# Kernel tuning notes

Measured on AMD Instinct MI355X. Metric: run time of the kernel, lower is better.

Reference implementation:

```python
import jax, jax.numpy as jnp
import numpy as np

_PI = np.pi

def _fibonacci_sphere(n):
    i = np.arange(n, dtype=np.float64)
    y = 1.0 - (i / float(n - 1)) * 2.0
    r = np.sqrt(np.maximum(1.0 - y * y, 0.0))
    theta = _PI * (3.0 - np.sqrt(5.0)) * i
    return np.stack([np.cos(theta) * r, y, np.sin(theta) * r], -1).astype(np.float32)

def _normalize(v, eps=1e-12):
    n = jnp.linalg.norm(v, axis=-1, keepdims=True)
    return v / jnp.maximum(n, eps)

def _sh4(v):
    # l=4 real spherical harmonics, orthonormal ('integral') normalization, 9 comps m=-4..4
    v = _normalize(v)
    x, y, z = v[..., 0], v[..., 1], v[..., 2]
    x2, y2, z2 = x * x, y * y, z * z
    c_m4 = 0.75 * np.sqrt(35.0 / _PI)
    c_m3 = 0.75 * np.sqrt(35.0 / (2.0 * _PI))
    c_m2 = 0.75 * np.sqrt(5.0 / _PI)
    c_m1 = 0.75 * np.sqrt(5.0 / (2.0 * _PI))
    c_0  = (3.0 / 16.0) * np.sqrt(1.0 / _PI)
    c_p2 = (3.0 / 8.0) * np.sqrt(5.0 / _PI)
    c_p4 = (3.0 / 16.0) * np.sqrt(35.0 / _PI)
    return jnp.stack([
        c_m4 * x * y * (x2 - y2),
        c_m3 * y * z * (3.0 * x2 - y2),
        c_m2 * x * y * (7.0 * z2 - 1.0),
        c_m1 * y * z * (7.0 * z2 - 3.0),
        c_0 * (35.0 * z2 * z2 - 30.0 * z2 + 3.0),
        c_m1 * x * z * (7.0 * z2 - 3.0),
        c_p2 * (x2 - y2) * (7.0 * z2 - 1.0),
        c_m3 * x * z * (x2 - y2),
        c_p4 * (x2 * x2 - 6.0 * x2 * y2 + y2 * y2),
    ], axis=-1)

def _matrix_to_quaternion(m):
    # pytorch3d-style robust conversion, m: [..., 3, 3], returns (w, x, y, z)
    m00, m01, m02 = m[..., 0, 0], m[..., 0, 1], m[..., 0, 2]
    m10, m11, m12 = m[..., 1, 0], m[..., 1, 1], m[..., 1, 2]
    m20, m21, m22 = m[..., 2, 0], m[..., 2, 1], m[..., 2, 2]
    q_abs = jnp.sqrt(jnp.maximum(jnp.stack([
        1.0 + m00 + m11 + m22,
        1.0 + m00 - m11 - m22,
        1.0 - m00 + m11 - m22,
        1.0 - m00 - m11 + m22,
    ], -1), 0.0))
    c0 = jnp.stack([q_abs[..., 0] ** 2, m21 - m12, m02 - m20, m10 - m01], -1)
    c1 = jnp.stack([m21 - m12, q_abs[..., 1] ** 2, m10 + m01, m02 + m20], -1)
    c2 = jnp.stack([m02 - m20, m10 + m01, q_abs[..., 2] ** 2, m12 + m21], -1)
    c3 = jnp.stack([m10 - m01, m20 + m02, m21 + m12, q_abs[..., 3] ** 2], -1)
    cand = jnp.stack([c0, c1, c2, c3], -2) / (2.0 * jnp.maximum(q_abs, 0.1))[..., None]
    best = jnp.argmax(q_abs, axis=-1)
    return jnp.take_along_axis(cand, best[..., None, None], axis=-2)[..., 0, :]

def setup_inputs() -> dict:
    key = jax.random.key(0)
    k0, k1, k4, k6 = jax.random.split(key, 4)
    B = 16384
    return {
        "f0": jax.random.normal(k0, (B, 1), dtype=jnp.float32),
        "f1": jax.random.normal(k1, (B, 3), dtype=jnp.float32),
        "f4": jax.random.normal(k4, (B, 9), dtype=jnp.float32),
        "f6": jax.random.normal(k6, (B, 13), dtype=jnp.float32),
        "grid_vecs": jnp.asarray(_fibonacci_sphere(10000)),
    }

def reference(f0, f1, f4, f6, grid_vecs):
    Y4 = _sh4(grid_vecs)                               # [G, 9]
    signal = jnp.einsum('bi,gi->bg', f4, Y4)           # [B, G]  (memory-bound skinny matmul)
    z_idx = jnp.argmax(signal, axis=1)
    z_axis = grid_vecs[z_idx]                          # [B, 3]
    dots = jnp.einsum('bi,gi->bg', z_axis, grid_vecs)  # [B, G]
    masked = jnp.where(jnp.abs(dots) < 0.2, signal, -jnp.inf)
    x_idx = jnp.argmax(masked, axis=1)
    x_axis = grid_vecs[x_idx]
    z_axis = _normalize(z_axis)
    proj = jnp.sum(x_axis * z_axis, -1, keepdims=True) * z_axis
    x_axis = _normalize(x_axis - proj)
    y_axis = jnp.cross(z_axis, x_axis)
    R = jnp.stack([x_axis, y_axis, z_axis], axis=-1)   # axes as columns
    q_rec = _matrix_to_quaternion(R)                   # [B, 4]
    boundary_map = f0 * (180.0 / _PI)
    return q_rec, boundary_map
```

## Files before the change

kernel.cpp:

```cpp
#include <hip/hip_runtime.h>
#include <math.h>
#include <stdint.h>

#define NB 16384
#define NG 10000
#define NGT 313
#define NCH 20
#define MAXTPC 16

typedef _Float16 half4 __attribute__((ext_vector_type(4)));
typedef _Float16 half8 __attribute__((ext_vector_type(8)));
typedef float    floatx16 __attribute__((ext_vector_type(16)));

#define ROWMAP(r, kh) (((r) & 3) + 8 * ((r) >> 2) + 4 * (kh))

__device__ inline float max3f(float a, float b, float c) {
    float d;
    asm("v_max3_f32 %0, %1, %2, %3" : "=v"(d) : "v"(a), "v"(b), "v"(c));
    return d;
}

#define PACKF(p_, c_, F_) \
    asm("v_and_or_b32 %0, %1, %2, " F_ : "=v"(p_) : "v"(c_), "s"(mskc))

__device__ inline void stage_sh(const float* __restrict__ gv, half4* lds4, int t0, int nt) {
    const int nrows = nt * 32;
    for (int lr = threadIdx.x; lr < nrows; lr += 256) {
        int g = t0 * 32 + lr;
        half4 s0, s1, s2, s3;
        if (g >= NG) {
            const _Float16 qn = (_Float16)__builtin_nanf("");
            s0 = (half4){qn, qn, qn, qn}; s1 = s0; s2 = s0; s3 = s0;
        } else {
            float x = gv[3 * g + 0], y = gv[3 * g + 1], z = gv[3 * g + 2];
            float n2 = x * x + y * y + z * z;
            float rn = __frsqrt_rn(fmaxf(n2, 1e-24f));
            float vx = x * rn, vy = y * rn, vz = z * rn;
            float x2 = vx * vx, y2 = vy * vy, z2 = vz * vz;
            const float c_m4 = (float)(0.75 * sqrt(35.0 / M_PI));
            const float c_m3 = (float)(0.75 * sqrt(35.0 / (2.0 * M_PI)));
            const float c_m2 = (float)(0.75 * sqrt(5.0 / M_PI));
            const float c_m1 = (float)(0.75 * sqrt(5.0 / (2.0 * M_PI)));
            const float c_0  = (float)((3.0 / 16.0) * sqrt(1.0 / M_PI));
            const float c_p2 = (float)((3.0 / 8.0) * sqrt(5.0 / M_PI));
            const float c_p4 = (float)((3.0 / 16.0) * sqrt(35.0 / M_PI));
            s0[0] = (_Float16)(c_m4 * vx * vy * (x2 - y2));
            s0[1] = (_Float16)(c_m3 * vy * vz * (3.0f * x2 - y2));
            s0[2] = (_Float16)(c_m2 * vx * vy * (7.0f * z2 - 1.0f));
            s0[3] = (_Float16)(c_m1 * vy * vz * (7.0f * z2 - 3.0f));
            s1[0] = (_Float16)(c_0  * (35.0f * z2 * z2 - 30.0f * z2 + 3.0f));
            s1[1] = (_Float16)(c_m1 * vx * vz * (7.0f * z2 - 3.0f));
            s1[2] = (_Float16)(c_p2 * (x2 - y2) * (7.0f * z2 - 1.0f));
            s1[3] = (_Float16)(c_m3 * vx * vz * (x2 - y2));
            s2[0] = (_Float16)(c_p4 * (x2 * x2 - 6.0f * x2 * y2 + y2 * y2));
            s2[1] = (_Float16)x;
            s2[2] = (_Float16)y;
            s2[3] = (_Float16)z;
            s3 = (half4){0, 0, 0, 0};
        }
        half4* row = lds4 + lr * 5;
        row[0] = s0; row[1] = s1; row[2] = s2; row[3] = s3;
    }
}

__device__ inline half8 make_bfrag(const float* __restrict__ f4, int b, int kh) {
    half8 a = {0, 0, 0, 0, 0, 0, 0, 0};
    const float* fr = f4 + (size_t)b * 9;
    if (kh == 0) {
#pragma unroll
        for (int j = 0; j < 8; ++j) a[j] = (_Float16)fr[j];
    } else {
        a[0] = (_Float16)fr[8];
    }
    return a;
}

__device__ inline void merge_vg(float& v, int& g, float v2, int g2) {
    bool take = (v2 > v) || (v2 == v && g2 < g);
    v = take ? v2 : v;
    g = take ? g2 : g;
}

__global__ __launch_bounds__(256, 6) void k_pass1(const float* __restrict__ f4,
                                                  const float* __restrict__ gv,
                                                  float* __restrict__ Pv,
                                                  int* __restrict__ Pi) {
    __shared__ half4 lds4[MAXTPC * 32 * 5];
    const int lane = threadIdx.x & 63;
    const int w = threadIdx.x >> 6;
    const int W = blockIdx.x * 4 + w;
    const int n = lane & 31, kh = lane >> 5;
    const int chunk = blockIdx.y;
    const int b = W * 32 + n;

    const int t0 = (NGT * chunk) / NCH;
    const int t1 = (NGT * (chunk + 1)) / NCH;
    const int nt = t1 - t0;

    stage_sh(gv, lds4, t0, nt);
    const half8 bf = make_bfrag(f4, b, kh);
    __syncthreads();

    const floatx16 zero16 = {0.f,0.f,0.f,0.f, 0.f,0.f,0.f,0.f, 0.f,0.f,0.f,0.f, 0.f,0.f,0.f,0.f};
    const unsigned mskc = 0xFFFFFFF0u;
    float run = -INFINITY; int bt = 0;

    const half4* lp = lds4 + n * 5 + kh * 2;
    half4 a0 = lp[0], a1 = lp[1]; lp += 32 * 5;

    for (int t = 0; t < nt - 1; ++t) {
        half4 b0 = lp[0], b1 = lp[1]; lp += 32 * 5;
        half8 af = __builtin_shufflevector(a0, a1, 0, 1, 2, 3, 4, 5, 6, 7);
        floatx16 c = __builtin_amdgcn_mfma_f32_32x32x16_f16(af, bf, zero16, 0, 0, 0);
        float p0,p1,p2,p3,p4,p5,p6,p7,p8,p9,p10,p11,p12,p13,p14,p15;
        PACKF(p0,  c[0],  "15"); PACKF(p1,  c[1],  "14");
        PACKF(p2,  c[2],  "13"); PACKF(p3,  c[3],  "12");
        PACKF(p4,  c[4],  "11"); PACKF(p5,  c[5],  "10");
        PACKF(p6,  c[6],  "9");  PACKF(p7,  c[7],  "8");
        PACKF(p8,  c[8],  "7");  PACKF(p9,  c[9],  "6");
        PACKF(p10, c[10], "5");  PACKF(p11, c[11], "4");
        PACKF(p12, c[12], "3");  PACKF(p13, c[13], "2");
        PACKF(p14, c[14], "1");  PACKF(p15, c[15], "0");
        float u0 = max3f(p0, p1, p2);
        float u1 = max3f(p3, p4, p5);
        float u2 = max3f(p6, p7, p8);
        float u3 = max3f(p9, p10, p11);
        float u4 = max3f(p12, p13, p14);
        float u5 = max3f(u0, u1, p15);
        float u6 = max3f(u2, u3, u4);
        float tm = fmaxf(u5, u6);
        bt = (tm > run) ? t : bt;
        run = fmaxf(run, tm);
        a0 = b0; a1 = b1;
    }
    {
        half8 af = __builtin_shufflevector(a0, a1, 0, 1, 2, 3, 4, 5, 6, 7);
        floatx16 c = __builtin_amdgcn_mfma_f32_32x32x16_f16(af, bf, zero16, 0, 0, 0);
        if (chunk == NCH - 1) {
#pragma unroll
            for (int r = 0; r < 16; ++r) c[r] = fmaxf(c[r], -3.0e38f);
        }
        float p0,p1,p2,p3,p4,p5,p6,p7,p8,p9,p10,p11,p12,p13,p14,p15;
        PACKF(p0,  c[0],  "15"); PACKF(p1,  c[1],  "14");
        PACKF(p2,  c[2],  "13"); PACKF(p3,  c[3],  "12");
        PACKF(p4,  c[4],  "11"); PACKF(p5,  c[5],  "10");
        PACKF(p6,  c[6],  "9");  PACKF(p7,  c[7],  "8");
        PACKF(p8,  c[8],  "7");  PACKF(p9,  c[9],  "6");
        PACKF(p10, c[10], "5");  PACKF(p11, c[11], "4");
        PACKF(p12, c[12], "3");  PACKF(p13, c[13], "2");
        PACKF(p14, c[14], "1");  PACKF(p15, c[15], "0");
        float u0 = max3f(p0, p1, p2);
        float u1 = max3f(p3, p4, p5);
        float u2 = max3f(p6, p7, p8);
        float u3 = max3f(p9, p10, p11);
        float u4 = max3f(p12, p13, p14);
        float u5 = max3f(u0, u1, p15);
        float u6 = max3f(u2, u3, u4);
        float tm = fmaxf(u5, u6);
        bt = (tm > run) ? (nt - 1) : bt;
        run = fmaxf(run, tm);
    }
    unsigned rb = __float_as_uint(run);
    int rwin = 15 - (int)(rb & 15u);
    int row = ROWMAP(rwin, kh);
    float v = __uint_as_float(rb & 0xFFFFFFF0u);
    int g = (t0 + bt) * 32 + row;
    merge_vg(v, g, __shfl_xor(v, 32), __shfl_xor(g, 32));
    if (kh == 0) {
        Pv[(size_t)chunk * NB + b] = v;
        Pi[(size_t)chunk * NB + b] = g;
    }
}

__global__ __launch_bounds__(256) void k_zred(const float* __restrict__ P1v,
                                              const int* __restrict__ P1i,
                                              const float* __restrict__ gv,
                                              float* __restrict__ zax) {
    const int b = blockIdx.x * 256 + threadIdx.x;
    float bz = -INFINITY; int zi = 0;
#pragma unroll
    for (int cc = 0; cc < NCH; ++cc) {
        float v = P1v[(size_t)cc * NB + b];
        int   i = P1i[(size_t)cc * NB + b];
        if (v > bz || (v == bz && i < zi)) { bz = v; zi = i; }
    }
    float4 z4 = {gv[3 * zi + 0], gv[3 * zi + 1], gv[3 * zi + 2], 0.f};
    *(float4*)(zax + 4 * (size_t)b) = z4;
}

__global__ __launch_bounds__(256, 6) void k_pass2(const float* __restrict__ f4,
                                                  const float* __restrict__ gv,
                                                  const float* __restrict__ zax,
                                                  float* __restrict__ P2v,
                                                  int* __restrict__ P2i) {
    __shared__ half4 lds4[MAXTPC * 32 * 5];
    const int lane = threadIdx.x & 63;
    const int w = threadIdx.x >> 6;
    const int W = blockIdx.x * 4 + w;
    const int n = lane & 31, kh = lane >> 5;
    const int chunk = blockIdx.y;
    const int b = W * 32 + n;

    const int t0 = (NGT * chunk) / NCH;
    const int t1 = (NGT * (chunk + 1)) / NCH;
    const int nt = t1 - t0;

    stage_sh(gv, lds4, t0, nt);
    const half8 bf = make_bfrag(f4, b, kh);
    half8 df = {0, 0, 0, 0, 0, 0, 0, 0};
    if (kh == 1) {
        const float* zp = zax + 4 * (size_t)b;
        df[1] = (_Float16)zp[0];
        df[2] = (_Float16)zp[1];
        df[3] = (_Float16)zp[2];
    }
    __syncthreads();

    const floatx16 zero16 = {0.f,0.f,0.f,0.f, 0.f,0.f,0.f,0.f, 0.f,0.f,0.f,0.f, 0.f,0.f,0.f,0.f};
    const unsigned mskc = 0xFFFFFFF0u;
    const float ninf = -INFINITY;
    const float lim = 0.2f;
    float run = -INFINITY; int bt = 0;

    const half4* lp = lds4 + n * 5 + kh * 2;
    half4 a0 = lp[0], a1 = lp[1]; lp += 32 * 5;

    for (int t = 0; t < nt; ++t) {
        half4 b0, b1;
        if (t < nt - 1) { b0 = lp[0]; b1 = lp[1]; lp += 32 * 5; }
        half8 af = __builtin_shufflevector(a0, a1, 0, 1, 2, 3, 4, 5, 6, 7);
        floatx16 cs = __builtin_amdgcn_mfma_f32_32x32x16_f16(af, bf, zero16, 0, 0, 0);
        floatx16 cd = __builtin_amdgcn_mfma_f32_32x32x16_f16(af, df, zero16, 0, 0, 0);
        float q;
        float s0,s1,s2,s3,s4,s5,s6,s7,s8,s9,s10,s11,s12,s13,s14,s15;
        PACKF(q, cs[0],  "15"); s0  = (fabsf(cd[0])  < lim) ? q : ninf;
        PACKF(q, cs[1],  "14"); s1  = (fabsf(cd[1])  < lim) ? q : ninf;
        PACKF(q, cs[2],  "13"); s2  = (fabsf(cd[2])  < lim) ? q : ninf;
        PACKF(q, cs[3],  "12"); s3  = (fabsf(cd[3])  < lim) ? q : ninf;
        PACKF(q, cs[4],  "11"); s4  = (fabsf(cd[4])  < lim) ? q : ninf;
        PACKF(q, cs[5],  "10"); s5  = (fabsf(cd[5])  < lim) ? q : ninf;
        PACKF(q, cs[6],  "9");  s6  = (fabsf(cd[6])  < lim) ? q : ninf;
        PACKF(q, cs[7],  "8");  s7  = (fabsf(cd[7])  < lim) ? q : ninf;
        PACKF(q, cs[8],  "7");  s8  = (fabsf(cd[8])  < lim) ? q : ninf;
        PACKF(q, cs[9],  "6");  s9  = (fabsf(cd[9])  < lim) ? q : ninf;
        PACKF(q, cs[10], "5");  s10 = (fabsf(cd[10]) < lim) ? q : ninf;
        PACKF(q, cs[11], "4");  s11 = (fabsf(cd[11]) < lim) ? q : ninf;
        PACKF(q, cs[12], "3");  s12 = (fabsf(cd[12]) < lim) ? q : ninf;
        PACKF(q, cs[13], "2");  s13 = (fabsf(cd[13]) < lim) ? q : ninf;
        PACKF(q, cs[14], "1");  s14 = (fabsf(cd[14]) < lim) ? q : ninf;
        PACKF(q, cs[15], "0");  s15 = (fabsf(cd[15]) < lim) ? q : ninf;
        float u0 = max3f(s0, s1, s2);
        float u1 = max3f(s3, s4, s5);
        float u2 = max3f(s6, s7, s8);
        float u3 = max3f(s9, s10, s11);
        float u4 = max3f(s12, s13, s14);
        float u5 = max3f(u0, u1, s15);
        float u6 = max3f(u2, u3, u4);
        float tm = fmaxf(u5, u6);
        bt = (tm > run) ? t : bt;
        run = fmaxf(run, tm);
        a0 = b0; a1 = b1;
    }
    unsigned rb = __float_as_uint(run);
    int rwin = 15 - (int)(rb & 15u);
    int row = ROWMAP(rwin, kh);
    float v = __uint_as_float(rb & 0xFFFFFFF0u);
    int g = (t0 + bt) * 32 + row;
    merge_vg(v, g, __shfl_xor(v, 32), __shfl_xor(g, 32));
    if (kh == 0) {
        P2v[(size_t)chunk * NB + b] = v;
        P2i[(size_t)chunk * NB + b] = g;
    }
}

__global__ __launch_bounds__(256) void k_final(const float* __restrict__ f0,
                                               const float* __restrict__ gv,
                                               const float* __restrict__ zax,
                                               const float* __restrict__ P2v,
                                               const int* __restrict__ P2i,
                                               float* __restrict__ out) {
    int b = blockIdx.x * 256 + threadIdx.x;
    float bx = -INFINITY; int xi = 0;
#pragma unroll
    for (int cc = 0; cc < NCH; ++cc) {
        float v = P2v[(size_t)cc * NB + b];
        int   i = P2i[(size_t)cc * NB + b];
        if (v > bx || (v == bx && i < xi)) { bx = v; xi = i; }
    }
    const float* zp = zax + 4 * (size_t)b;
    float zr0 = zp[0], zr1 = zp[1], zr2 = zp[2];
    float xr0 = gv[3 * xi], xr1 = gv[3 * xi + 1], xr2 = gv[3 * xi + 2];
    float zn = sqrtf(zr0 * zr0 + zr1 * zr1 + zr2 * zr2);
    float zd = fmaxf(zn, 1e-12f);
    float z0 = zr0 / zd, z1 = zr1 / zd, z2 = zr2 / zd;
    float pr = xr0 * z0 + xr1 * z1 + xr2 * z2;
    float ux = xr0 - pr * z0, uy = xr1 - pr * z1, uz = xr2 - pr * z2;
    float xn = sqrtf(ux * ux + uy * uy + uz * uz);
    float xd = fmaxf(xn, 1e-12f);
    float x0 = ux / xd, x1 = uy / xd, x2 = uz / xd;
    float y0 = z1 * x2 - z2 * x1;
    float y1 = z2 * x0 - z0 * x2;
    float y2 = z0 * x1 - z1 * x0;
    float m00 = x0, m01 = y0, m02 = z0;
    float m10 = x1, m11 = y1, m12 = z1;
    float m20 = x2, m21 = y2, m22 = z2;
    float q0 = sqrtf(fmaxf(1.0f + m00 + m11 + m22, 0.0f));
    float q1 = sqrtf(fmaxf(1.0f + m00 - m11 - m22, 0.0f));
    float q2 = sqrtf(fmaxf(1.0f - m00 + m11 - m22, 0.0f));
    float q3 = sqrtf(fmaxf(1.0f - m00 - m11 + m22, 0.0f));
    int bq = 0; float qb = q0;
    if (q1 > qb) { qb = q1; bq = 1; }
    if (q2 > qb) { qb = q2; bq = 2; }
    if (q3 > qb) { qb = q3; bq = 3; }
    float dd = 2.0f * fmaxf(qb, 0.1f);
    float wq, qx, qy, qz;
    if (bq == 0)      { wq = q0 * q0;  qx = m21 - m12; qy = m02 - m20; qz = m10 - m01; }
    else if (bq == 1) { wq = m21 - m12; qx = q1 * q1;  qy = m10 + m01; qz = m02 + m20; }
    else if (bq == 2) { wq = m02 - m20; qx = m10 + m01; qy = q2 * q2;  qz = m12 + m21; }
    else              { wq = m10 - m01; qx = m20 + m02; qy = m21 + m12; qz = q3 * q3; }
    out[b * 4 + 0] = wq / dd;
    out[b * 4 + 1] = qx / dd;
    out[b * 4 + 2] = qy / dd;
    out[b * 4 + 3] = qz / dd;
    out[4 * NB + b] = f0[b] * (float)(180.0 / M_PI);
}

extern "C" void kernel_launch(void* const* d_in, const int* in_sizes, int n_in,
                              void* d_out, int out_size, void* d_ws, size_t ws_size,
                              hipStream_t stream) {
    const float* f0 = (const float*)d_in[0];
    const float* f4 = (const float*)d_in[2];
    const float* gv = (const float*)d_in[4];
    float* out = (float*)d_out;
    (void)in_sizes; (void)n_in; (void)out_size; (void)ws_size;

    char* W = (char*)d_ws;
    float* P1v = (float*)(W + 0);
    int*   P1i = (int*)(W + 0x180000);
    float* P2v = (float*)(W + 2 * 0x180000);
    int*   P2i = (int*)(W + 3 * 0x180000);
    float* zax = (float*)(W + 4 * 0x180000);

    dim3 grid2(128, NCH);
    k_pass1<<<grid2, 256, 0, stream>>>(f4, gv, P1v, P1i);
    k_zred<<<NB / 256, 256, 0, stream>>>(P1v, P1i, gv, zax);
    k_pass2<<<grid2, 256, 0, stream>>>(f4, gv, zax, P2v, P2i);
    k_final<<<NB / 256, 256, 0, stream>>>(f0, gv, zax, P2v, P2i, out);
}
```

Before: 116.2 us.

## Fuse cross-chunk argmax reductions into pass kernels via last-block atomic counters

```diff
diff --git a/kernel.cpp b/kernel.cpp
--- a/kernel.cpp
+++ b/kernel.cpp
@@ -22,6 +22,19 @@
 
 #define PACKF(p_, c_, F_) \
     asm("v_and_or_b32 %0, %1, %2, " F_ : "=v"(p_) : "v"(c_), "s"(mskc))
+
+__device__ inline void  pst_f(float* p, size_t i, float v) {
+    __hip_atomic_store(p + i, v, __ATOMIC_RELAXED, __HIP_MEMORY_SCOPE_AGENT);
+}
+__device__ inline void  pst_i(int* p, size_t i, int v) {
+    __hip_atomic_store(p + i, v, __ATOMIC_RELAXED, __HIP_MEMORY_SCOPE_AGENT);
+}
+__device__ inline float pld_f(const float* p, size_t i) {
+    return __hip_atomic_load(p + i, __ATOMIC_RELAXED, __HIP_MEMORY_SCOPE_AGENT);
+}
+__device__ inline int   pld_i(const int* p, size_t i) {
+    return __hip_atomic_load(p + i, __ATOMIC_RELAXED, __HIP_MEMORY_SCOPE_AGENT);
+}
 
 __device__ inline void stage_sh(const float* __restrict__ gv, half4* lds4, int t0, int nt) {
     const int nrows = nt * 32;
@@ -81,10 +94,24 @@
     g = take ? g2 : g;
 }
 
+__device__ inline bool last_block_flag(unsigned long long* ctr, int* flag) {
+    __syncthreads();
+    if (threadIdx.x == 0) {
+        unsigned long long old = __hip_atomic_fetch_add(ctr + blockIdx.x, 1ull,
+                                                        __ATOMIC_ACQ_REL,
+                                                        __HIP_MEMORY_SCOPE_AGENT);
+        *flag = ((unsigned)(old % NCH) == NCH - 1);
+    }
+    __syncthreads();
+    return *flag != 0;
+}
+
 __global__ __launch_bounds__(256, 6) void k_pass1(const float* __restrict__ f4,
                                                   const float* __restrict__ gv,
-                                                  float* __restrict__ Pv,
-                                                  int* __restrict__ Pi) {
+                                                  float* __restrict__ P1v,
+                                                  int* __restrict__ P1i,
+                                                  float* __restrict__ zax,
+                                                  unsigned long long* ctr1) {
     __shared__ half4 lds4[MAXTPC * 32 * 5];
     const int lane = threadIdx.x & 63;
     const int w = threadIdx.x >> 6;
@@ -167,32 +194,32 @@
     int g = (t0 + bt) * 32 + row;
     merge_vg(v, g, __shfl_xor(v, 32), __shfl_xor(g, 32));
     if (kh == 0) {
-        Pv[(size_t)chunk * NB + b] = v;
-        Pi[(size_t)chunk * NB + b] = g;
-    }
-}
-
-__global__ __launch_bounds__(256) void k_zred(const float* __restrict__ P1v,
-                                              const int* __restrict__ P1i,
-                                              const float* __restrict__ gv,
-                                              float* __restrict__ zax) {
-    const int b = blockIdx.x * 256 + threadIdx.x;
-    float bz = -INFINITY; int zi = 0;
+        pst_f(P1v, (size_t)chunk * NB + b, v);
+        pst_i(P1i, (size_t)chunk * NB + b, g);
+    }
+
+    if (last_block_flag(ctr1, (int*)lds4) && threadIdx.x < 128) {
+        const int b2 = blockIdx.x * 128 + threadIdx.x;
+        float bz = -INFINITY; int zi = 0;
 #pragma unroll
-    for (int cc = 0; cc < NCH; ++cc) {
-        float v = P1v[(size_t)cc * NB + b];
-        int   i = P1i[(size_t)cc * NB + b];
-        if (v > bz || (v == bz && i < zi)) { bz = v; zi = i; }
-    }
-    float4 z4 = {gv[3 * zi + 0], gv[3 * zi + 1], gv[3 * zi + 2], 0.f};
-    *(float4*)(zax + 4 * (size_t)b) = z4;
-}
-
-__global__ __launch_bounds__(256, 6) void k_pass2(const float* __restrict__ f4,
+        for (int cc = 0; cc < NCH; ++cc) {
+            float vv = pld_f(P1v, (size_t)cc * NB + b2);
+            int   ii = pld_i(P1i, (size_t)cc * NB + b2);
+            merge_vg(bz, zi, vv, ii);
+        }
+        float4 z4 = {gv[3 * zi + 0], gv[3 * zi + 1], gv[3 * zi + 2], 0.f};
+        *(float4*)(zax + 4 * (size_t)b2) = z4;
+    }
+}
+
+__global__ __launch_bounds__(256, 6) void k_pass2(const float* __restrict__ f0,
+                                                  const float* __restrict__ f4,
                                                   const float* __restrict__ gv,
                                                   const float* __restrict__ zax,
                                                   float* __restrict__ P2v,
-                                                  int* __restrict__ P2i) {
+                                                  int* __restrict__ P2i,
+                                                  unsigned long long* ctr2,
+                                                  float* __restrict__ out) {
     __shared__ half4 lds4[MAXTPC * 32 * 5];
     const int lane = threadIdx.x & 63;
     const int w = threadIdx.x >> 6;
@@ -268,61 +295,56 @@
     int g = (t0 + bt) * 32 + row;
     merge_vg(v, g, __shfl_xor(v, 32), __shfl_xor(g, 32));
     if (kh == 0) {
-        P2v[(size_t)chunk * NB + b] = v;
-        P2i[(size_t)chunk * NB + b] = g;
-    }
-}
-
-__global__ __launch_bounds__(256) void k_final(const float* __restrict__ f0,
-                                               const float* __restrict__ gv,
-                                               const float* __restrict__ zax,
-                                               const float* __restrict__ P2v,
-                                               const int* __restrict__ P2i,
-                                               float* __restrict__ out) {
-    int b = blockIdx.x * 256 + threadIdx.x;
-    float bx = -INFINITY; int xi = 0;
+        pst_f(P2v, (size_t)chunk * NB + b, v);
+        pst_i(P2i, (size_t)chunk * NB + b, g);
+    }
+
+    if (last_block_flag(ctr2, (int*)lds4) && threadIdx.x < 128) {
+        const int b2 = blockIdx.x * 128 + threadIdx.x;
+        float bx = -INFINITY; int xi = 0;
 #pragma unroll
-    for (int cc = 0; cc < NCH; ++cc) {
-        float v = P2v[(size_t)cc * NB + b];
-        int   i = P2i[(size_t)cc * NB + b];
-        if (v > bx || (v == bx && i < xi)) { bx = v; xi = i; }
-    }
-    const float* zp = zax + 4 * (size_t)b;
-    float zr0 = zp[0], zr1 = zp[1], zr2 = zp[2];
-    float xr0 = gv[3 * xi], xr1 = gv[3 * xi + 1], xr2 = gv[3 * xi + 2];
-    float zn = sqrtf(zr0 * zr0 + zr1 * zr1 + zr2 * zr2);
-    float zd = fmaxf(zn, 1e-12f);
-    float z0 = zr0 / zd, z1 = zr1 / zd, z2 = zr2 / zd;
-    float pr = xr0 * z0 + xr1 * z1 + xr2 * z2;
-    float ux = xr0 - pr * z0, uy = xr1 - pr * z1, uz = xr2 - pr * z2;
-    float xn = sqrtf(ux * ux + uy * uy + uz * uz);
-    float xd = fmaxf(xn, 1e-12f);
-    float x0 = ux / xd, x1 = uy / xd, x2 = uz / xd;
-    float y0 = z1 * x2 - z2 * x1;
-    float y1 = z2 * x0 - z0 * x2;
-    float y2 = z0 * x1 - z1 * x0;
-    float m00 = x0, m01 = y0, m02 = z0;
-    float m10 = x1, m11 = y1, m12 = z1;
-    float m20 = x2, m21 = y2, m22 = z2;
-    float q0 = sqrtf(fmaxf(1.0f + m00 + m11 + m22, 0.0f));
-    float q1 = sqrtf(fmaxf(1.0f + m00 - m11 - m22, 0.0f));
-    float q2 = sqrtf(fmaxf(1.0f - m00 + m11 - m22, 0.0f));
-    float q3 = sqrtf(fmaxf(1.0f - m00 - m11 + m22, 0.0f));
-    int bq = 0; float qb = q0;
-    if (q1 > qb) { qb = q1; bq = 1; }
-    if (q2 > qb) { qb = q2; bq = 2; }
-    if (q3 > qb) { qb = q3; bq = 3; }
-    float dd = 2.0f * fmaxf(qb, 0.1f);
-    float wq, qx, qy, qz;
-    if (bq == 0)      { wq = q0 * q0;  qx = m21 - m12; qy = m02 - m20; qz = m10 - m01; }
-    else if (bq == 1) { wq = m21 - m12; qx = q1 * q1;  qy = m10 + m01; qz = m02 + m20; }
-    else if (bq == 2) { wq = m02 - m20; qx = m10 + m01; qy = q2 * q2;  qz = m12 + m21; }
-    else              { wq = m10 - m01; qx = m20 + m02; qy = m21 + m12; qz = q3 * q3; }
-    out[b * 4 + 0] = wq / dd;
-    out[b * 4 + 1] = qx / dd;
-    out[b * 4 + 2] = qy / dd;
-    out[b * 4 + 3] = qz / dd;
-    out[4 * NB + b] = f0[b] * (float)(180.0 / M_PI);
+        for (int cc = 0; cc < NCH; ++cc) {
+            float vv = pld_f(P2v, (size_t)cc * NB + b2);
+            int   ii = pld_i(P2i, (size_t)cc * NB + b2);
+            merge_vg(bx, xi, vv, ii);
+        }
+        const float* zp = zax + 4 * (size_t)b2;
+        float zr0 = zp[0], zr1 = zp[1], zr2 = zp[2];
+        float xr0 = gv[3 * xi], xr1 = gv[3 * xi + 1], xr2 = gv[3 * xi + 2];
+        float zn = sqrtf(zr0 * zr0 + zr1 * zr1 + zr2 * zr2);
+        float zd = fmaxf(zn, 1e-12f);
+        float z0 = zr0 / zd, z1 = zr1 / zd, z2 = zr2 / zd;
+        float pr = xr0 * z0 + xr1 * z1 + xr2 * z2;
+        float ux = xr0 - pr * z0, uy = xr1 - pr * z1, uz = xr2 - pr * z2;
+        float xn = sqrtf(ux * ux + uy * uy + uz * uz);
+        float xd = fmaxf(xn, 1e-12f);
+        float x0 = ux / xd, x1 = uy / xd, x2 = uz / xd;
+        float y0 = z1 * x2 - z2 * x1;
+        float y1 = z2 * x0 - z0 * x2;
+        float y2 = z0 * x1 - z1 * x0;
+        float m00 = x0, m01 = y0, m02 = z0;
+        float m10 = x1, m11 = y1, m12 = z1;
+        float m20 = x2, m21 = y2, m22 = z2;
+        float q0 = sqrtf(fmaxf(1.0f + m00 + m11 + m22, 0.0f));
+        float q1 = sqrtf(fmaxf(1.0f + m00 - m11 - m22, 0.0f));
+        float q2 = sqrtf(fmaxf(1.0f - m00 + m11 - m22, 0.0f));
+        float q3 = sqrtf(fmaxf(1.0f - m00 - m11 + m22, 0.0f));
+        int bq = 0; float qb = q0;
+        if (q1 > qb) { qb = q1; bq = 1; }
+        if (q2 > qb) { qb = q2; bq = 2; }
+        if (q3 > qb) { qb = q3; bq = 3; }
+        float dd = 2.0f * fmaxf(qb, 0.1f);
+        float wq, qx, qy, qz;
+        if (bq == 0)      { wq = q0 * q0;  qx = m21 - m12; qy = m02 - m20; qz = m10 - m01; }
+        else if (bq == 1) { wq = m21 - m12; qx = q1 * q1;  qy = m10 + m01; qz = m02 + m20; }
+        else if (bq == 2) { wq = m02 - m20; qx = m10 + m01; qy = q2 * q2;  qz = m12 + m21; }
+        else              { wq = m10 - m01; qx = m20 + m02; qy = m21 + m12; qz = q3 * q3; }
+        out[b2 * 4 + 0] = wq / dd;
+        out[b2 * 4 + 1] = qx / dd;
+        out[b2 * 4 + 2] = qy / dd;
+        out[b2 * 4 + 3] = qz / dd;
+        out[4 * NB + b2] = f0[b2] * (float)(180.0 / M_PI);
+    }
 }
 
 extern "C" void kernel_launch(void* const* d_in, const int* in_sizes, int n_in,
@@ -340,10 +362,10 @@
     float* P2v = (float*)(W + 2 * 0x180000);
     int*   P2i = (int*)(W + 3 * 0x180000);
     float* zax = (float*)(W + 4 * 0x180000);
+    unsigned long long* ctr1 = (unsigned long long*)(W + 5 * 0x180000);
+    unsigned long long* ctr2 = (unsigned long long*)(W + 5 * 0x180000 + 4096);
 
     dim3 grid2(128, NCH);
-    k_pass1<<<grid2, 256, 0, stream>>>(f4, gv, P1v, P1i);
-    k_zred<<<NB / 256, 256, 0, stream>>>(P1v, P1i, gv, zax);
-    k_pass2<<<grid2, 256, 0, stream>>>(f4, gv, zax, P2v, P2i);
-    k_final<<<NB / 256, 256, 0, stream>>>(f0, gv, zax, P2v, P2i, out);
-}
+    k_pass1<<<grid2, 256, 0, stream>>>(f4, gv, P1v, P1i, zax, ctr1);
+    k_pass2<<<grid2, 256, 0, stream>>>(f0, f4, gv, zax, P2v, P2i, ctr2, out);
+}
```

New measurement: 162.1 us. +39.5%, slower.
